# Performance work log

Measured on AMD Instinct MI355X. Metric: run time of the kernel, lower is better.

The kernel has to match this reference:

```python
import jax, jax.numpy as jnp
import numpy as np
from jax import lax

EPS = 1e-15
MAX_TANH = 1.0 - 1e-5


def _artanh(x):
    x = jnp.clip(x, -MAX_TANH, MAX_TANH)
    return jnp.arctanh(x)


def mobius_add(x, y):
    # Poincare ball, c=1 (geoopt create_ball default)
    x2 = jnp.sum(x * x, axis=-1, keepdims=True)
    y2 = jnp.sum(y * y, axis=-1, keepdims=True)
    xy = jnp.sum(x * y, axis=-1, keepdims=True)
    num = (1.0 + 2.0 * xy + y2) * x + (1.0 - x2) * y
    den = 1.0 + 2.0 * xy + x2 * y2
    return num / jnp.maximum(den, EPS)


def mobius_matvec(x, W):
    # geoopt: mobius_matvec(weight.T, x) == hyperbolic version of x @ W
    x_norm = jnp.maximum(jnp.linalg.norm(x, axis=-1, keepdims=True), EPS)
    mx = x @ W
    mx_norm = jnp.maximum(jnp.linalg.norm(mx, axis=-1, keepdims=True), EPS)
    res = jnp.tanh(mx_norm / x_norm * _artanh(x_norm)) * (mx / mx_norm)
    return jnp.where(mx_norm <= 1e-10, jnp.zeros_like(res), res)


def logmap0(y):
    yn = jnp.maximum(jnp.linalg.norm(y, axis=-1, keepdims=True), EPS)
    return _artanh(yn) * y / yn


def expmap0(u):
    un = jnp.maximum(jnp.linalg.norm(u, axis=-1, keepdims=True), EPS)
    return jnp.tanh(un) * u / un


def setup_inputs() -> dict:
    key = jax.random.key(0)
    k1, k2, k3, k4 = jax.random.split(key, 4)
    N, IN, OUT, DEG = 20000, 512, 256, 16
    feat = jax.random.normal(k1, (N, IN), dtype=jnp.float32) * 0.02    # points near origin of ball
    weight = jax.random.normal(k2, (IN, OUT), dtype=jnp.float32) * (1.0 / np.sqrt(IN))
    bias = jax.random.normal(k3, (OUT,), dtype=jnp.float32) * 0.01
    src = jax.random.randint(k4, (N, DEG), 0, N, dtype=jnp.int32)      # in-neighbors per node
    return {"feat": feat, "weight": weight, "bias": bias, "src": src}


def reference(feat, weight, bias, src):
    N, deg = src.shape
    norm = jnp.asarray(deg, feat.dtype) ** -0.5  # in_degrees == deg for all nodes
    h = feat * norm
    # in_feats > out_feats branch: transform before aggregation
    h = mobius_matvec(h, weight)                 # [N, OUT]
    msgs = h[src]                                # gather mailbox [N, deg, OUT]
    # sequential left-fold with mobius_add over neighbors (non-associative)
    carry = msgs[:, 0]
    rest = jnp.moveaxis(msgs[:, 1:], 1, 0)       # [deg-1, N, OUT]

    def step(c, m):
        return mobius_add(c, m), None

    rst, _ = lax.scan(step, carry, rest)
    rst = rst * norm
    rst = mobius_add(rst, bias)
    rst = expmap0(jax.nn.relu(logmap0(rst)))     # hyperbolic relu
    return rst
```

## Files before the change

kernel.cpp:

```cpp
#include <hip/hip_runtime.h>
#include <hip/hip_fp16.h>
#include <math.h>

#define EPSF 1e-15f
#define MAX_TANH_F (1.0f - 1e-5f)
#define KDIM 512
#define NOUT 256
#define BM 32
#define BK 64

#define BAR_LDS() asm volatile("s_waitcnt lgkmcnt(0)\n\ts_barrier" ::: "memory")

typedef __attribute__((ext_vector_type(8))) __bf16 bf16x8;
typedef __attribute__((ext_vector_type(4))) float f32x4;

__device__ __forceinline__ float artanh_clip(float x) {
    x = fminf(fmaxf(x, -MAX_TANH_F), MAX_TANH_F);
    return atanhf(x);
}

__device__ __forceinline__ void unpack2h(unsigned int u, float& a, float& b) {
    __half2 h = __builtin_bit_cast(__half2, u);
    a = __low2float(h);
    b = __high2float(h);
}

__device__ __forceinline__ bf16x8 cvt8(const float4& a, const float4& b) {
    bf16x8 r;
    r[0] = (__bf16)a.x; r[1] = (__bf16)a.y; r[2] = (__bf16)a.z; r[3] = (__bf16)a.w;
    r[4] = (__bf16)b.x; r[5] = (__bf16)b.y; r[6] = (__bf16)b.z; r[7] = (__bf16)b.w;
    return r;
}
__device__ __forceinline__ float sq8(const float4& a, const float4& b) {
    return a.x*a.x + a.y*a.y + a.z*a.z + a.w*a.w
         + b.x*b.x + b.y*b.y + b.z*b.z + b.w*b.w;
}

__global__ __launch_bounds__(64) void prep_w_kernel(
    const float* __restrict__ W, unsigned int* __restrict__ Wp)
{
    const int b = blockIdx.x;
    const int l = threadIdx.x;
    const int k0 = (b >> 4) * 32 + (l >> 4) * 8;
    const int col = (b & 15) * 16 + (l & 15);
    bf16x8 v;
    #pragma unroll
    for (int j = 0; j < 8; ++j) v[j] = (__bf16)W[(size_t)(k0 + j) * NOUT + col];
    *(uint4*)(Wp + ((size_t)b * 64 + l) * 4) = __builtin_bit_cast(uint4, v);
}

__global__ __launch_bounds__(256) void gemm_mobius_kernel(
    const float* __restrict__ feat, const uint4* __restrict__ Wp,
    __half* __restrict__ h, float* __restrict__ hnorm2,
    float scale, int N)
{
    __shared__ float lds_a[2][BM * BK];
    __shared__ float sred[4][BM];
    __shared__ float sfac[BM];
    __shared__ float sxn2[BM];

    const int tid  = threadIdx.x;
    const int wave = tid >> 6;
    const int lane = tid & 63;
    const int rr   = lane & 15;
    const int g    = lane >> 4;
    const int base = blockIdx.x * BM;

    const int srow = tid >> 3;
    const int sk   = (tid & 7) * 8;
    const int grow = base + srow;
    const float* gsrc = feat + (size_t)(grow < N ? grow : N - 1) * KDIM + sk;
    const int wslot0 = (((tid & 7) * 2)     ^ (srow & 15)) * 4;
    const int wslot1 = (((tid & 7) * 2 + 1) ^ (srow & 15)) * 4;

    f32x4 acc[2][4];
    #pragma unroll
    for (int hh = 0; hh < 2; ++hh)
        #pragma unroll
        for (int t = 0; t < 4; ++t) acc[hh][t] = (f32x4){0.f, 0.f, 0.f, 0.f};

    const uint4* wp = Wp + (size_t)wave * 4 * 64 + lane;

    uint4 B[2][4];
    #pragma unroll
    for (int p = 0; p < 2; ++p)
        #pragma unroll
        for (int t = 0; t < 4; ++t)
            B[p][t] = wp[((size_t)p * 16 + t) * 64];

    float4 t0a = *(const float4*)(gsrc);
    float4 t0b = *(const float4*)(gsrc + 4);
    float4 navOa = *(const float4*)(gsrc + 1 * BK);
    float4 navOb = *(const float4*)(gsrc + 1 * BK + 4);
    float4 navEa = *(const float4*)(gsrc + 2 * BK);
    float4 navEb = *(const float4*)(gsrc + 2 * BK + 4);
    {
        float* d = &lds_a[0][srow * BK];
        *(float4*)(d + wslot0) = t0a;
        *(float4*)(d + wslot1) = t0b;
    }
    BAR_LDS();

    float xs0 = 0.f, xs1 = 0.f;

    #pragma unroll
    for (int kk = 0; kk < 8; ++kk) {
        if (kk < 7) {
            float* d = &lds_a[(kk + 1) & 1][srow * BK];
            if ((kk & 1) == 0) {
                *(float4*)(d + wslot0) = navOa;
                *(float4*)(d + wslot1) = navOb;
                if (kk + 3 < 8) {
                    navOa = *(const float4*)(gsrc + (kk + 3) * BK);
                    navOb = *(const float4*)(gsrc + (kk + 3) * BK + 4);
                }
            } else {
                *(float4*)(d + wslot0) = navEa;
                *(float4*)(d + wslot1) = navEb;
                if (kk + 3 < 8) {
                    navEa = *(const float4*)(gsrc + (kk + 3) * BK);
                    navEb = *(const float4*)(gsrc + (kk + 3) * BK + 4);
                }
            }
        }

        const float* buf = lds_a[kk & 1];
        #pragma unroll
        for (int ss = 0; ss < 2; ++ss) {
            const int s = kk * 2 + ss;
            const int ls0 = ((ss * 8 + g * 2)     ^ rr) * 4;
            const int ls1 = ((ss * 8 + g * 2 + 1) ^ rr) * 4;
            float4 a00 = *(const float4*)(buf + rr * BK + ls0);
            float4 a01 = *(const float4*)(buf + rr * BK + ls1);
            float4 a10 = *(const float4*)(buf + (16 + rr) * BK + ls0);
            float4 a11 = *(const float4*)(buf + (16 + rr) * BK + ls1);
            xs0 += sq8(a00, a01);
            xs1 += sq8(a10, a11);
            bf16x8 ah0 = cvt8(a00, a01);
            bf16x8 ah1 = cvt8(a10, a11);
            uint4 b0 = B[s & 1][0], b1 = B[s & 1][1], b2 = B[s & 1][2], b3 = B[s & 1][3];
            if (s + 2 < 16) {
                #pragma unroll
                for (int t = 0; t < 4; ++t)
                    B[s & 1][t] = wp[((size_t)(s + 2) * 16 + t) * 64];
            }
            acc[0][0] = __builtin_amdgcn_mfma_f32_16x16x32_bf16(ah0, __builtin_bit_cast(bf16x8, b0), acc[0][0], 0, 0, 0);
            acc[1][0] = __builtin_amdgcn_mfma_f32_16x16x32_bf16(ah1, __builtin_bit_cast(bf16x8, b0), acc[1][0], 0, 0, 0);
            acc[0][1] = __builtin_amdgcn_mfma_f32_16x16x32_bf16(ah0, __builtin_bit_cast(bf16x8, b1), acc[0][1], 0, 0, 0);
            acc[1][1] = __builtin_amdgcn_mfma_f32_16x16x32_bf16(ah1, __builtin_bit_cast(bf16x8, b1), acc[1][1], 0, 0, 0);
            acc[0][2] = __builtin_amdgcn_mfma_f32_16x16x32_bf16(ah0, __builtin_bit_cast(bf16x8, b2), acc[0][2], 0, 0, 0);
            acc[1][2] = __builtin_amdgcn_mfma_f32_16x16x32_bf16(ah1, __builtin_bit_cast(bf16x8, b2), acc[1][2], 0, 0, 0);
            acc[0][3] = __builtin_amdgcn_mfma_f32_16x16x32_bf16(ah0, __builtin_bit_cast(bf16x8, b3), acc[0][3], 0, 0, 0);
            acc[1][3] = __builtin_amdgcn_mfma_f32_16x16x32_bf16(ah1, __builtin_bit_cast(bf16x8, b3), acc[1][3], 0, 0, 0);
        }
        BAR_LDS();
    }

    xs0 += __shfl_xor(xs0, 16); xs0 += __shfl_xor(xs0, 32);
    xs1 += __shfl_xor(xs1, 16); xs1 += __shfl_xor(xs1, 32);
    if (wave == 0 && lane < 16) { sxn2[lane] = xs0; sxn2[16 + lane] = xs1; }

    #pragma unroll
    for (int hh = 0; hh < 2; ++hh) {
        #pragma unroll
        for (int r = 0; r < 4; ++r) {
            float p = 0.f;
            #pragma unroll
            for (int t = 0; t < 4; ++t) p += acc[hh][t][r] * acc[hh][t][r];
            p += __shfl_xor(p, 1);
            p += __shfl_xor(p, 2);
            p += __shfl_xor(p, 4);
            p += __shfl_xor(p, 8);
            if (rr == 0) sred[wave][hh * 16 + g * 4 + r] = p;
        }
    }
    __syncthreads();

    if (tid < BM) {
        const int r = tid;
        const float mx2 = sred[0][r] + sred[1][r] + sred[2][r] + sred[3][r];
        const float mxn = fmaxf(scale * sqrtf(mx2), EPSF);
        const float xn  = fmaxf(scale * sqrtf(sxn2[r]), EPSF);
        float ttv = tanhf(mxn / xn * artanh_clip(xn));
        float fc  = ttv * scale / mxn;
        if (mxn <= 1e-10f) { fc = 0.f; ttv = 0.f; }
        sfac[r] = fc;
        if (base + r < N) hnorm2[base + r] = ttv * ttv;
    }
    __syncthreads();

    #pragma unroll
    for (int hh = 0; hh < 2; ++hh) {
        #pragma unroll
        for (int r = 0; r < 4; ++r) {
            const int row_r = base + hh * 16 + g * 4 + r;
            if (row_r < N) {
                const float fc = sfac[hh * 16 + g * 4 + r];
                __half* hr = h + (size_t)row_r * NOUT + wave * 64 + rr;
                #pragma unroll
                for (int t = 0; t < 4; ++t) hr[t * 16] = __float2half(acc[hh][t][r] * fc);
            }
        }
    }
}

__global__ __launch_bounds__(256) void aggregate_kernel(
    const __half* __restrict__ h, const float* __restrict__ hnorm2,
    const int* __restrict__ src, const float* __restrict__ bias,
    float* __restrict__ out, float scale, int N)
{
    const int wave = threadIdx.x >> 6;
    const int lane = threadIdx.x & 63;
    const int n0 = (blockIdx.x * 4 + wave) * 4;
    if (n0 >= N) return;
    const int g = lane >> 4;
    const int q = lane & 15;
    const int myrow = n0 + g;
    const bool rowok = myrow < N;

    size_t smax = (size_t)N * 16 - 1;
    size_t soff = (size_t)n0 * 16 + lane;
    int sidx = src[soff <= smax ? soff : smax];
    float y2v = hnorm2[sidx];

    int idx[16];
    float y2[16];
    #pragma unroll
    for (int j = 0; j < 16; ++j) {
        idx[j] = __shfl(sidx, (lane & 48) + j);
        y2[j]  = __shfl(y2v, (lane & 48) + j);
    }

    uint4 cur0, cur1;
    {
        const uint4* hp = (const uint4*)(h + (size_t)idx[0] * NOUT);
        cur0 = hp[q * 2]; cur1 = hp[q * 2 + 1];
    }
    uint4 pa[4], pb[4];
    #pragma unroll
    for (int p = 0; p < 4; ++p) {
        const uint4* hp = (const uint4*)(h + (size_t)idx[p + 1] * NOUT);
        pa[p] = hp[q * 2]; pb[p] = hp[q * 2 + 1];
    }

    float c[16];
    unpack2h(cur0.x, c[0], c[1]);   unpack2h(cur0.y, c[2], c[3]);
    unpack2h(cur0.z, c[4], c[5]);   unpack2h(cur0.w, c[6], c[7]);
    unpack2h(cur1.x, c[8], c[9]);   unpack2h(cur1.y, c[10], c[11]);
    unpack2h(cur1.z, c[12], c[13]); unpack2h(cur1.w, c[14], c[15]);
    float c2 = y2[0];

    #pragma unroll
    for (int j = 1; j < 16; ++j) {
        const int slot = (j - 1) & 3;
        uint4 p0 = pa[slot], p1 = pb[slot];
        if (j + 4 < 16) {
            const uint4* hp = (const uint4*)(h + (size_t)idx[j + 4] * NOUT);
            pa[slot] = hp[q * 2]; pb[slot] = hp[q * 2 + 1];
        }
        float yv[16];
        unpack2h(p0.x, yv[0], yv[1]);   unpack2h(p0.y, yv[2], yv[3]);
        unpack2h(p0.z, yv[4], yv[5]);   unpack2h(p0.w, yv[6], yv[7]);
        unpack2h(p1.x, yv[8], yv[9]);   unpack2h(p1.y, yv[10], yv[11]);
        unpack2h(p1.z, yv[12], yv[13]); unpack2h(p1.w, yv[14], yv[15]);

        float xp = 0.f;
        #pragma unroll
        for (int i = 0; i < 16; ++i) xp = fmaf(c[i], yv[i], xp);
        xp += __shfl_xor(xp, 1);
        xp += __shfl_xor(xp, 2);
        xp += __shfl_xor(xp, 4);
        xp += __shfl_xor(xp, 8);
        const float xy = xp;

        const float A = 1.f + 2.f * xy + y2[j];
        const float B = 1.f - c2;
        const float den = fmaxf(1.f + 2.f * xy + c2 * y2[j], EPSF);
        const float inv = __builtin_amdgcn_rcpf(den);
        #pragma unroll
        for (int i = 0; i < 16; ++i) c[i] = (fmaf(A, c[i], B * yv[i])) * inv;
        c2 = fmaxf((A * A * c2 + 2.f * A * B * xy + B * B * y2[j]) * (inv * inv), 0.f);
    }

    #pragma unroll
    for (int i = 0; i < 16; ++i) c[i] *= scale;
    c2 *= scale * scale;

    float bv[16];
    {
        const float4* bp = (const float4*)(bias + q * 16);
        float4 b0 = bp[0], b1 = bp[1], b2 = bp[2], b3 = bp[3];
        bv[0]=b0.x; bv[1]=b0.y; bv[2]=b0.z; bv[3]=b0.w;
        bv[4]=b1.x; bv[5]=b1.y; bv[6]=b1.z; bv[7]=b1.w;
        bv[8]=b2.x; bv[9]=b2.y; bv[10]=b2.z; bv[11]=b2.w;
        bv[12]=b3.x; bv[13]=b3.y; bv[14]=b3.z; bv[15]=b3.w;
    }
    float bp_ = 0.f, xp_ = 0.f;
    #pragma unroll
    for (int i = 0; i < 16; ++i) { bp_ = fmaf(bv[i], bv[i], bp_); xp_ = fmaf(c[i], bv[i], xp_); }
    bp_ += __shfl_xor(bp_, 1); xp_ += __shfl_xor(xp_, 1);
    bp_ += __shfl_xor(bp_, 2); xp_ += __shfl_xor(xp_, 2);
    bp_ += __shfl_xor(bp_, 4); xp_ += __shfl_xor(xp_, 4);
    bp_ += __shfl_xor(bp_, 8); xp_ += __shfl_xor(xp_, 8);
    const float bb = bp_, xy = xp_;

    const float A = 1.f + 2.f * xy + bb;
    const float B = 1.f - c2;
    const float den = fmaxf(1.f + 2.f * xy + c2 * bb, EPSF);
    const float inv = 1.f / den;
    float r4[16];
    #pragma unroll
    for (int i = 0; i < 16; ++i) r4[i] = fmaf(A, c[i], B * bv[i]) * inv;
    const float rn2 = fmaxf((A * A * c2 + 2.f * A * B * xy + B * B * bb) * (inv * inv), 0.f);

    const float rn = fmaxf(sqrtf(rn2), EPSF);
    const float lf = artanh_clip(rn) / rn;
    float u[16];
    float up = 0.f;
    #pragma unroll
    for (int i = 0; i < 16; ++i) { u[i] = fmaxf(r4[i] * lf, 0.f); up = fmaf(u[i], u[i], up); }
    up += __shfl_xor(up, 1);
    up += __shfl_xor(up, 2);
    up += __shfl_xor(up, 4);
    up += __shfl_xor(up, 8);
    const float un = fmaxf(sqrtf(up), EPSF);
    const float ef = tanhf(un) / un;

    if (rowok) {
        float* op = out + (size_t)myrow * NOUT + q * 16;
        float4 o;
        o.x = u[0]*ef;  o.y = u[1]*ef;  o.z = u[2]*ef;  o.w = u[3]*ef;  ((float4*)op)[0] = o;
        o.x = u[4]*ef;  o.y = u[5]*ef;  o.z = u[6]*ef;  o.w = u[7]*ef;  ((float4*)op)[1] = o;
        o.x = u[8]*ef;  o.y = u[9]*ef;  o.z = u[10]*ef; o.w = u[11]*ef; ((float4*)op)[2] = o;
        o.x = u[12]*ef; o.y = u[13]*ef; o.z = u[14]*ef; o.w = u[15]*ef; ((float4*)op)[3] = o;
    }
}

extern "C" void kernel_launch(void* const* d_in, const int* in_sizes, int n_in,
                              void* d_out, int out_size, void* d_ws, size_t ws_size,
                              hipStream_t stream) {
    const float* feat   = (const float*)d_in[0];
    const float* weight = (const float*)d_in[1];
    const float* bias   = (const float*)d_in[2];
    const int*   src    = (const int*)d_in[3];

    const int OUT = in_sizes[2];
    const int IN  = in_sizes[1] / OUT;
    const int N   = in_sizes[0] / IN;
    const int DEG = in_sizes[3] / N;
    (void)IN; (void)DEG; (void)out_size; (void)ws_size; (void)n_in;

    const float scale = 1.0f / sqrtf((float)DEG);

    char* ws = (char*)d_ws;
    __half* h     = (__half*)ws;
    float* hnorm2 = (float*)(ws + (size_t)N * NOUT * 2);
    unsigned int* Wp = (unsigned int*)(ws + (size_t)N * NOUT * 2 + (size_t)N * 4);

    float* out = (float*)d_out;

    const int nbm = (N + BM - 1) / BM;

    hipLaunchKernelGGL(prep_w_kernel, dim3(256), dim3(64), 0, stream,
                       weight, Wp);
    hipLaunchKernelGGL(gemm_mobius_kernel, dim3(nbm), dim3(256), 0, stream,
                       feat, (const uint4*)Wp, h, hnorm2, scale, N);
    hipLaunchKernelGGL(aggregate_kernel, dim3((N + 15) / 16), dim3(256), 0, stream,
                       h, hnorm2, src, bias, out, scale, N);
}
```

Before: 52.09 us.

## Express mobius fold as linear combination using MFMA Gram matrix of neighbors

The aggregation kernel is rewritten so each wave handles one node. It computes the 16x16 Gram matrix of the neighbor features with f16 MFMA, then runs the sequential mobius-add fold only on scalar coefficients, since every carry is a linear combination of the neighbors. The final vector is rebuilt once as a weighted sum of neighbor rows. This removes the 15 serial full-vector updates and cross-lane dot products, but reads each neighbor row twice and reorders the floating-point accumulation.

```diff
diff --git a/kernel.cpp b/kernel.cpp
--- a/kernel.cpp
+++ b/kernel.cpp
@@ -12,6 +12,7 @@
 #define BAR_LDS() asm volatile("s_waitcnt lgkmcnt(0)\n\ts_barrier" ::: "memory")
 
 typedef __attribute__((ext_vector_type(8))) __bf16 bf16x8;
+typedef __attribute__((ext_vector_type(8))) _Float16 f16x8;
 typedef __attribute__((ext_vector_type(4))) float f32x4;
 
 __device__ __forceinline__ float artanh_clip(float x) {
@@ -20,9 +21,9 @@
 }
 
 __device__ __forceinline__ void unpack2h(unsigned int u, float& a, float& b) {
-    __half2 h = __builtin_bit_cast(__half2, u);
-    a = __low2float(h);
-    b = __high2float(h);
+    __half2 hh = __builtin_bit_cast(__half2, u);
+    a = __low2float(hh);
+    b = __high2float(hh);
 }
 
 __device__ __forceinline__ bf16x8 cvt8(const float4& a, const float4& b) {
@@ -211,129 +212,117 @@
 {
     const int wave = threadIdx.x >> 6;
     const int lane = threadIdx.x & 63;
-    const int n0 = (blockIdx.x * 4 + wave) * 4;
-    if (n0 >= N) return;
+    const int n = blockIdx.x * 4 + wave;
+    if (n >= N) return;
+    const int q = lane & 15;
     const int g = lane >> 4;
-    const int q = lane & 15;
-    const int myrow = n0 + g;
-    const bool rowok = myrow < N;
-
-    size_t smax = (size_t)N * 16 - 1;
-    size_t soff = (size_t)n0 * 16 + lane;
-    int sidx = src[soff <= smax ? soff : smax];
-    float y2v = hnorm2[sidx];
-
-    int idx[16];
-    float y2[16];
-    #pragma unroll
-    for (int j = 0; j < 16; ++j) {
-        idx[j] = __shfl(sidx, (lane & 48) + j);
-        y2[j]  = __shfl(y2v, (lane & 48) + j);
-    }
-
-    uint4 cur0, cur1;
-    {
-        const uint4* hp = (const uint4*)(h + (size_t)idx[0] * NOUT);
-        cur0 = hp[q * 2]; cur1 = hp[q * 2 + 1];
-    }
-    uint4 pa[4], pb[4];
-    #pragma unroll
-    for (int p = 0; p < 4; ++p) {
-        const uint4* hp = (const uint4*)(h + (size_t)idx[p + 1] * NOUT);
-        pa[p] = hp[q * 2]; pb[p] = hp[q * 2 + 1];
-    }
-
-    float c[16];
-    unpack2h(cur0.x, c[0], c[1]);   unpack2h(cur0.y, c[2], c[3]);
-    unpack2h(cur0.z, c[4], c[5]);   unpack2h(cur0.w, c[6], c[7]);
-    unpack2h(cur1.x, c[8], c[9]);   unpack2h(cur1.y, c[10], c[11]);
-    unpack2h(cur1.z, c[12], c[13]); unpack2h(cur1.w, c[14], c[15]);
-    float c2 = y2[0];
+
+    const int sidx = src[(size_t)n * 16 + q];
+    const float y2v = hnorm2[sidx];
+
+    const char* mrow = (const char*)(h + (size_t)sidx * NOUT) + g * 16;
+    uint4 f0 = *(const uint4*)(mrow + 0 * 64);
+    uint4 f1 = *(const uint4*)(mrow + 1 * 64);
+    uint4 f2 = *(const uint4*)(mrow + 2 * 64);
+    uint4 f3 = *(const uint4*)(mrow + 3 * 64);
+    uint4 f4 = *(const uint4*)(mrow + 4 * 64);
+    uint4 f5 = *(const uint4*)(mrow + 5 * 64);
+    uint4 f6 = *(const uint4*)(mrow + 6 * 64);
+    uint4 f7 = *(const uint4*)(mrow + 7 * 64);
+
+    f32x4 Gm = (f32x4){0.f, 0.f, 0.f, 0.f};
+    Gm = __builtin_amdgcn_mfma_f32_16x16x32_f16(__builtin_bit_cast(f16x8, f0), __builtin_bit_cast(f16x8, f0), Gm, 0, 0, 0);
+    Gm = __builtin_amdgcn_mfma_f32_16x16x32_f16(__builtin_bit_cast(f16x8, f1), __builtin_bit_cast(f16x8, f1), Gm, 0, 0, 0);
+    Gm = __builtin_amdgcn_mfma_f32_16x16x32_f16(__builtin_bit_cast(f16x8, f2), __builtin_bit_cast(f16x8, f2), Gm, 0, 0, 0);
+    Gm = __builtin_amdgcn_mfma_f32_16x16x32_f16(__builtin_bit_cast(f16x8, f3), __builtin_bit_cast(f16x8, f3), Gm, 0, 0, 0);
+    Gm = __builtin_amdgcn_mfma_f32_16x16x32_f16(__builtin_bit_cast(f16x8, f4), __builtin_bit_cast(f16x8, f4), Gm, 0, 0, 0);
+    Gm = __builtin_amdgcn_mfma_f32_16x16x32_f16(__builtin_bit_cast(f16x8, f5), __builtin_bit_cast(f16x8, f5), Gm, 0, 0, 0);
+    Gm = __builtin_amdgcn_mfma_f32_16x16x32_f16(__builtin_bit_cast(f16x8, f6), __builtin_bit_cast(f16x8, f6), Gm, 0, 0, 0);
+    Gm = __builtin_amdgcn_mfma_f32_16x16x32_f16(__builtin_bit_cast(f16x8, f7), __builtin_bit_cast(f16x8, f7), Gm, 0, 0, 0);
+
+    float a0 = (g == 0) ? 1.f : 0.f;
+    float a1 = 0.f, a2 = 0.f, a3 = 0.f;
+    float c2 = __shfl(y2v, 0);
 
     #pragma unroll
     for (int j = 1; j < 16; ++j) {
-        const int slot = (j - 1) & 3;
-        uint4 p0 = pa[slot], p1 = pb[slot];
-        if (j + 4 < 16) {
-            const uint4* hp = (const uint4*)(h + (size_t)idx[j + 4] * NOUT);
-            pa[slot] = hp[q * 2]; pb[slot] = hp[q * 2 + 1];
-        }
-        float yv[16];
-        unpack2h(p0.x, yv[0], yv[1]);   unpack2h(p0.y, yv[2], yv[3]);
-        unpack2h(p0.z, yv[4], yv[5]);   unpack2h(p0.w, yv[6], yv[7]);
-        unpack2h(p1.x, yv[8], yv[9]);   unpack2h(p1.y, yv[10], yv[11]);
-        unpack2h(p1.z, yv[12], yv[13]); unpack2h(p1.w, yv[14], yv[15]);
-
-        float xp = 0.f;
-        #pragma unroll
-        for (int i = 0; i < 16; ++i) xp = fmaf(c[i], yv[i], xp);
-        xp += __shfl_xor(xp, 1);
-        xp += __shfl_xor(xp, 2);
-        xp += __shfl_xor(xp, 4);
-        xp += __shfl_xor(xp, 8);
-        const float xy = xp;
-
-        const float A = 1.f + 2.f * xy + y2[j];
-        const float B = 1.f - c2;
-        const float den = fmaxf(1.f + 2.f * xy + c2 * y2[j], EPSF);
+        float p = fmaf(a0, Gm[0], fmaf(a1, Gm[1], fmaf(a2, Gm[2], a3 * Gm[3])));
+        p += __shfl_xor(p, 16);
+        p += __shfl_xor(p, 32);
+        const float xy  = __shfl(p, j);
+        const float y2j = __shfl(y2v, j);
+        const float A = 1.f + 2.f * xy + y2j;
+        const float Bc = 1.f - c2;
+        const float den = fmaxf(1.f + 2.f * xy + c2 * y2j, EPSF);
         const float inv = __builtin_amdgcn_rcpf(den);
-        #pragma unroll
-        for (int i = 0; i < 16; ++i) c[i] = (fmaf(A, c[i], B * yv[i])) * inv;
-        c2 = fmaxf((A * A * c2 + 2.f * A * B * xy + B * B * y2[j]) * (inv * inv), 0.f);
-    }
-
-    #pragma unroll
-    for (int i = 0; i < 16; ++i) c[i] *= scale;
+        const float Ai = A * inv, Bi = Bc * inv;
+        a0 *= Ai; a1 *= Ai; a2 *= Ai; a3 *= Ai;
+        if (g == (j >> 2)) {
+            if ((j & 3) == 0)      a0 = Bi;
+            else if ((j & 3) == 1) a1 = Bi;
+            else if ((j & 3) == 2) a2 = Bi;
+            else                   a3 = Bi;
+        }
+        c2 = fmaxf((A * A * c2 + 2.f * A * Bc * xy + Bc * Bc * y2j) * (inv * inv), 0.f);
+    }
+
+    a0 *= scale; a1 *= scale; a2 *= scale; a3 *= scale;
     c2 *= scale * scale;
 
-    float bv[16];
-    {
-        const float4* bp = (const float4*)(bias + q * 16);
-        float4 b0 = bp[0], b1 = bp[1], b2 = bp[2], b3 = bp[3];
-        bv[0]=b0.x; bv[1]=b0.y; bv[2]=b0.z; bv[3]=b0.w;
-        bv[4]=b1.x; bv[5]=b1.y; bv[6]=b1.z; bv[7]=b1.w;
-        bv[8]=b2.x; bv[9]=b2.y; bv[10]=b2.z; bv[11]=b2.w;
-        bv[12]=b3.x; bv[13]=b3.y; bv[14]=b3.z; bv[15]=b3.w;
-    }
-    float bp_ = 0.f, xp_ = 0.f;
-    #pragma unroll
-    for (int i = 0; i < 16; ++i) { bp_ = fmaf(bv[i], bv[i], bp_); xp_ = fmaf(c[i], bv[i], xp_); }
-    bp_ += __shfl_xor(bp_, 1); xp_ += __shfl_xor(xp_, 1);
-    bp_ += __shfl_xor(bp_, 2); xp_ += __shfl_xor(xp_, 2);
-    bp_ += __shfl_xor(bp_, 4); xp_ += __shfl_xor(xp_, 4);
-    bp_ += __shfl_xor(bp_, 8); xp_ += __shfl_xor(xp_, 8);
-    const float bb = bp_, xy = xp_;
-
+    float cv0 = 0.f, cv1 = 0.f, cv2 = 0.f, cv3 = 0.f;
+    #pragma unroll
+    for (int q2 = 0; q2 < 16; ++q2) {
+        const int srcl = (q2 >> 2) * 16;
+        float aq;
+        if ((q2 & 3) == 0)      aq = __shfl(a0, srcl);
+        else if ((q2 & 3) == 1) aq = __shfl(a1, srcl);
+        else if ((q2 & 3) == 2) aq = __shfl(a2, srcl);
+        else                    aq = __shfl(a3, srcl);
+        const int iq = __shfl(sidx, q2);
+        const uint2 hv = *(const uint2*)(h + (size_t)iq * NOUT + lane * 4);
+        float w0, w1, w2, w3;
+        unpack2h(hv.x, w0, w1);
+        unpack2h(hv.y, w2, w3);
+        cv0 = fmaf(aq, w0, cv0);
+        cv1 = fmaf(aq, w1, cv1);
+        cv2 = fmaf(aq, w2, cv2);
+        cv3 = fmaf(aq, w3, cv3);
+    }
+
+    const float4 b4 = *(const float4*)(bias + lane * 4);
+    float bp = b4.x*b4.x + b4.y*b4.y + b4.z*b4.z + b4.w*b4.w;
+    float xp = cv0*b4.x + cv1*b4.y + cv2*b4.z + cv3*b4.w;
+    #pragma unroll
+    for (int d = 1; d < 64; d <<= 1) {
+        bp += __shfl_xor(bp, d);
+        xp += __shfl_xor(xp, d);
+    }
+    const float bb = bp, xy = xp;
     const float A = 1.f + 2.f * xy + bb;
-    const float B = 1.f - c2;
+    const float Bc = 1.f - c2;
     const float den = fmaxf(1.f + 2.f * xy + c2 * bb, EPSF);
     const float inv = 1.f / den;
-    float r4[16];
-    #pragma unroll
-    for (int i = 0; i < 16; ++i) r4[i] = fmaf(A, c[i], B * bv[i]) * inv;
-    const float rn2 = fmaxf((A * A * c2 + 2.f * A * B * xy + B * B * bb) * (inv * inv), 0.f);
+    float r0 = fmaf(A, cv0, Bc * b4.x) * inv;
+    float r1 = fmaf(A, cv1, Bc * b4.y) * inv;
+    float r2 = fmaf(A, cv2, Bc * b4.z) * inv;
+    float r3 = fmaf(A, cv3, Bc * b4.w) * inv;
+    const float rn2 = fmaxf((A * A * c2 + 2.f * A * Bc * xy + Bc * Bc * bb) * (inv * inv), 0.f);
 
     const float rn = fmaxf(sqrtf(rn2), EPSF);
     const float lf = artanh_clip(rn) / rn;
-    float u[16];
-    float up = 0.f;
-    #pragma unroll
-    for (int i = 0; i < 16; ++i) { u[i] = fmaxf(r4[i] * lf, 0.f); up = fmaf(u[i], u[i], up); }
-    up += __shfl_xor(up, 1);
-    up += __shfl_xor(up, 2);
-    up += __shfl_xor(up, 4);
-    up += __shfl_xor(up, 8);
+    float u0 = fmaxf(r0 * lf, 0.f);
+    float u1 = fmaxf(r1 * lf, 0.f);
+    float u2 = fmaxf(r2 * lf, 0.f);
+    float u3 = fmaxf(r3 * lf, 0.f);
+    float up = u0*u0 + u1*u1 + u2*u2 + u3*u3;
+    #pragma unroll
+    for (int d = 1; d < 64; d <<= 1) up += __shfl_xor(up, d);
     const float un = fmaxf(sqrtf(up), EPSF);
     const float ef = tanhf(un) / un;
 
-    if (rowok) {
-        float* op = out + (size_t)myrow * NOUT + q * 16;
-        float4 o;
-        o.x = u[0]*ef;  o.y = u[1]*ef;  o.z = u[2]*ef;  o.w = u[3]*ef;  ((float4*)op)[0] = o;
-        o.x = u[4]*ef;  o.y = u[5]*ef;  o.z = u[6]*ef;  o.w = u[7]*ef;  ((float4*)op)[1] = o;
-        o.x = u[8]*ef;  o.y = u[9]*ef;  o.z = u[10]*ef; o.w = u[11]*ef; ((float4*)op)[2] = o;
-        o.x = u[12]*ef; o.y = u[13]*ef; o.z = u[14]*ef; o.w = u[15]*ef; ((float4*)op)[3] = o;
-    }
+    float4 o;
+    o.x = u0 * ef; o.y = u1 * ef; o.z = u2 * ef; o.w = u3 * ef;
+    *(float4*)(out + (size_t)n * NOUT + lane * 4) = o;
 }
 
 extern "C" void kernel_launch(void* const* d_in, const int* in_sizes, int n_in,
@@ -365,6 +354,6 @@
                        weight, Wp);
     hipLaunchKernelGGL(gemm_mobius_kernel, dim3(nbm), dim3(256), 0, stream,
                        feat, (const uint4*)Wp, h, hnorm2, scale, N);
-    hipLaunchKernelGGL(aggregate_kernel, dim3((N + 15) / 16), dim3(256), 0, stream,
+    hipLaunchKernelGGL(aggregate_kernel, dim3((N + 3) / 4), dim3(256), 0, stream,
                        h, hnorm2, src, bias, out, scale, N);
 }
```

Measured after the change: 64.95 us. 24.7% more time.
